# Kernel optimization log

Measured on AMD Instinct MI355X. Metric: run time of the kernel, lower is better.

The kernel has to match this reference:

```python
import jax, jax.numpy as jnp
import numpy as np

B, L, D_MODEL, D_FF, H = 2, 2048, 512, 512, 8
DK = D_FF // H


def _lin(key, fan_in, fan_out):
    k1, k2 = jax.random.split(key)
    lim = 1.0 / np.sqrt(fan_in)
    W = jax.random.uniform(k1, (fan_in, fan_out), jnp.float32, -lim, lim)
    b = jax.random.uniform(k2, (fan_out,), jnp.float32, -lim, lim)
    return W, b


def setup_inputs() -> dict:
    key = jax.random.key(0)
    ks = jax.random.split(key, 13)
    x = jax.random.normal(ks[0], (B, L, D_MODEL), jnp.float32)
    x_knowledge = jax.random.normal(ks[1], (B, L, D_MODEL), jnp.float32)
    Wv, bv = _lin(ks[2], D_MODEL, D_FF)
    Wk, bk = _lin(ks[3], D_MODEL, D_FF)
    Wq, bq = _lin(ks[4], D_MODEL, D_FF)
    Wkf, bkf = _lin(ks[5], D_MODEL, D_FF)
    Wqf, bqf = _lin(ks[6], D_MODEL, D_FF)
    Wq2, bq2 = _lin(ks[7], D_FF, D_FF)
    Wk2, bk2 = _lin(ks[8], D_FF, D_FF)
    Wkf2, bkf2 = _lin(ks[9], D_FF, D_FF)
    Wqf2, bqf2 = _lin(ks[10], D_FF, D_FF)
    Wo, bo = _lin(ks[11], D_FF, D_MODEL)
    return dict(x=x, x_knowledge=x_knowledge, Wv=Wv, bv=bv, Wk=Wk, bk=bk,
                Wq=Wq, bq=bq, Wkf=Wkf, bkf=bkf, Wqf=Wqf, bqf=bqf,
                Wq2=Wq2, bq2=bq2, Wk2=Wk2, bk2=bk2, Wqf2=Wqf2, bqf2=bqf2,
                Wkf2=Wkf2, bkf2=bkf2, Wo=Wo, bo=bo)


def reference(x, x_knowledge, Wv, bv, Wk, bk, Wq, bq, Wkf, bkf, Wqf, bqf,
              Wq2, bq2, Wk2, bk2, Wqf2, bqf2, Wkf2, bkf2, Wo, bo):
    b, l, _ = x.shape
    # first projections from d_model -> d_ff
    v = x @ Wv + bv
    k = x @ Wk + bk
    q = x @ Wq + bq
    k_fei = x_knowledge @ Wkf + bkf
    q_fei = x_knowledge @ Wqf + bqf
    # second projections + NONSTANDARD head split: raw reshape (B,L,d_ff)->(B,h,L,dk)
    q = (q @ Wq2 + bq2).reshape(b, H, l, DK)
    k = (k @ Wk2 + bk2).reshape(b, H, l, DK)
    q_fei = (q_fei @ Wqf2 + bqf2).reshape(b, H, l, DK)
    k_fei = (k_fei @ Wkf2 + bkf2).reshape(b, H, l, DK)
    scale = 1.0 / np.sqrt(2.0 * DK).astype(np.float32)
    att = jnp.einsum('bhld,bhmd->bhlm', q, k) * scale
    att_fei = jnp.einsum('bhld,bhmd->bhlm', q_fei, k_fei) * scale
    score = jax.nn.softmax(att + att_fei, axis=-1)  # dropout is identity at eval
    v = v.reshape(b, H, l, DK)
    out = jnp.einsum('bhlm,bhmd->bhld', score, v).reshape(b, l, D_FF)
    return out @ Wo + bo
```

## Files before the change

kernel.cpp:

```cpp
#include <hip/hip_runtime.h>
#include <hip/hip_bf16.h>

typedef unsigned short u16;
typedef unsigned int   u32;
typedef __attribute__((ext_vector_type(8))) short bf16x8;
typedef __attribute__((ext_vector_type(4))) float f32x4;

#define SCALE 0.08838834764831845f
#define SCLOG 0.12752040542575836f

__device__ inline u16 f2bf(float f) {
  u32 u = __builtin_bit_cast(u32, f);
  u = (u + 0x7FFFu + ((u >> 16) & 1u)) >> 16;
  return (u16)u;
}
__device__ inline float bf2f(u16 b) {
  u32 u = (u32)b << 16;
  return __builtin_bit_cast(float, u);
}

__global__ __launch_bounds__(256) void cvt_bf16(const float* __restrict__ a,
                                                const float* __restrict__ b,
                                                u16* __restrict__ oa,
                                                u16* __restrict__ ob) {
  const float* in = blockIdx.y ? b : a;
  u16* out = blockIdx.y ? ob : oa;
  const int i = (blockIdx.x * 256 + threadIdx.x) * 8;
  float4 f0 = *(const float4*)(in + i);
  float4 f1 = *(const float4*)(in + i + 4);
  alignas(16) u16 t[8] = {f2bf(f0.x), f2bf(f0.y), f2bf(f0.z), f2bf(f0.w),
                          f2bf(f1.x), f2bf(f1.y), f2bf(f1.z), f2bf(f1.w)};
  *(uint4*)(out + i) = *(const uint4*)t;
}

struct TPtrs { const float* p[10]; };

__global__ __launch_bounds__(256) void transposeW(TPtrs ptrs, u16* __restrict__ out) {
  __shared__ u16 ts[64][65];
  const float sc = (blockIdx.z == 5 || blockIdx.z == 7) ? SCLOG : 1.0f;
  const float* in = ptrs.p[blockIdx.z];
  u16* o = out + (size_t)blockIdx.z * 262144;
  const int t = threadIdx.x;
  const int k0 = blockIdx.y * 64, n0 = blockIdx.x * 64;
  for (int pp = 0; pp < 16; ++pp) {
    int id = t + 256 * pp; int r = id >> 6, c = id & 63;
    ts[r][c] = f2bf(in[(size_t)(k0 + r) * 512 + n0 + c] * sc);
  }
  __syncthreads();
  for (int pp = 0; pp < 16; ++pp) {
    int id = t + 256 * pp; int r = id >> 6, c = id & 63;
    o[(size_t)(n0 + r) * 512 + k0 + c] = ts[c][r];
  }
}

struct BPtrs { const float* p[10]; };

__global__ __launch_bounds__(512) void biasPack(BPtrs bp, float* __restrict__ out) {
  const int z = blockIdx.x, n = threadIdx.x;
  const float sc = (z == 5 || z == 7) ? SCLOG : 1.0f;
  out[z * 512 + n] = bp.p[z][n] * sc;
}

__global__ __launch_bounds__(256) void transposeV(const u16* __restrict__ v1,
                                                  u16* __restrict__ vt) {
  __shared__ u16 ts[64][65];
  const size_t base = (size_t)blockIdx.y * 131072;
  const u16* in = v1 + base;
  u16* out = vt + base;
  const int l0 = blockIdx.x * 64;
  const int t = threadIdx.x;
  const int r = t >> 3, c8 = (t & 7) * 8;
  for (int pp = 0; pp < 2; ++pp) {
    int rr = r + pp * 32;
    *(uint4*)&ts[rr][c8] = *(const uint4*)&in[(size_t)(l0 + rr) * 64 + c8];
  }
  __syncthreads();
  for (int pp = 0; pp < 2; ++pp) {
    int d = r + pp * 32;
    alignas(16) u16 tmp[8];
    #pragma unroll
    for (int i = 0; i < 8; ++i) tmp[i] = ts[c8 + i][d];
    *(uint4*)&out[(size_t)d * 2048 + l0 + c8] = *(const uint4*)tmp;
  }
}

struct GemmBatch {
  const u16* A[4];
  const u16* Ax;
  int xsplit;
  void* out[5];
  int wrow0, zstride;
};

template <typename TOUT>
__global__ __launch_bounds__(256, 2) void gemm3(GemmBatch gb,
    const u16* __restrict__ Wt, const float* __restrict__ biasP) {
  const int tx = blockIdx.x, z = blockIdx.z;
  const u16* A = (tx < gb.xsplit) ? gb.A[z] : gb.Ax;
  const int wrow = gb.wrow0 + z * gb.zstride + tx * 128;
  const int m0 = blockIdx.y * 128;
  const u16* B = Wt + (size_t)wrow * 512;
  const float* bias = biasP + wrow;

  const int t = threadIdx.x, wid = t >> 6, lane = t & 63;
  const int lg = lane >> 4, ln = lane & 15;
  const int wr = wid >> 1, wc = wid & 1;

  __shared__ u16 As[2][128][64];
  __shared__ u16 Bs[2][128][64];

  const int srow = t >> 3, sch = t & 7;
  const int sw = (sch ^ (srow & 7)) * 8;
  const u16* Asrc = A + (size_t)(m0 + srow) * 512 + sch * 8;
  const u16* Bsrc = B + (size_t)srow * 512 + sch * 8;

  uint4 ra[4], rb[4];
  #pragma unroll
  for (int p = 0; p < 4; ++p) {
    ra[p] = *(const uint4*)(Asrc + p * 32 * 512);
    rb[p] = *(const uint4*)(Bsrc + p * 32 * 512);
  }
  #pragma unroll
  for (int p = 0; p < 4; ++p) {
    *(uint4*)&As[0][srow + 32 * p][sw] = ra[p];
    *(uint4*)&Bs[0][srow + 32 * p][sw] = rb[p];
  }
  __syncthreads();

  f32x4 acc[4][4];
  #pragma unroll
  for (int i = 0; i < 4; ++i)
    #pragma unroll
    for (int j = 0; j < 4; ++j)
      #pragma unroll
      for (int r = 0; r < 4; ++r) acc[i][j][r] = 0.0f;

  int cur = 0;
  for (int kt = 0; kt < 8; ++kt) {
    if (kt < 7) {
      const int ko = (kt + 1) * 64;
      #pragma unroll
      for (int p = 0; p < 4; ++p) {
        ra[p] = *(const uint4*)(Asrc + ko + p * 32 * 512);
        rb[p] = *(const uint4*)(Bsrc + ko + p * 32 * 512);
      }
    }
    #pragma unroll
    for (int ck = 0; ck < 2; ++ck) {
      bf16x8 af[4], bfr[4];
      #pragma unroll
      for (int mi = 0; mi < 4; ++mi) {
        const int r = wr * 64 + mi * 16 + ln;
        af[mi] = *(const bf16x8*)&As[cur][r][((ck * 4 + lg) ^ (r & 7)) * 8];
      }
      #pragma unroll
      for (int ni = 0; ni < 4; ++ni) {
        const int r = wc * 64 + ni * 16 + ln;
        bfr[ni] = *(const bf16x8*)&Bs[cur][r][((ck * 4 + lg) ^ (r & 7)) * 8];
      }
      #pragma unroll
      for (int mi = 0; mi < 4; ++mi)
        #pragma unroll
        for (int ni = 0; ni < 4; ++ni)
          acc[mi][ni] = __builtin_amdgcn_mfma_f32_16x16x32_bf16(
              af[mi], bfr[ni], acc[mi][ni], 0, 0, 0);
    }
    if (kt < 7) {
      #pragma unroll
      for (int p = 0; p < 4; ++p) {
        *(uint4*)&As[cur ^ 1][srow + 32 * p][sw] = ra[p];
        *(uint4*)&Bs[cur ^ 1][srow + 32 * p][sw] = rb[p];
      }
      __syncthreads();
      cur ^= 1;
    }
  }

  TOUT* C = (TOUT*)gb.out[(wrow >> 9) - (gb.wrow0 >> 9)];
  const int nbase = wrow & 511;
  #pragma unroll
  for (int ni = 0; ni < 4; ++ni) {
    const int colw = wc * 64 + ni * 16 + ln;
    const float bv = bias[colw];
    const int col = nbase + colw;
    #pragma unroll
    for (int mi = 0; mi < 4; ++mi)
      #pragma unroll
      for (int r = 0; r < 4; ++r) {
        const int row = m0 + wr * 64 + mi * 16 + 4 * lg + r;
        const float val = acc[mi][ni][r] + bv;
        if constexpr (sizeof(TOUT) == 4) C[(size_t)row * 512 + col] = val;
        else                             C[(size_t)row * 512 + col] = f2bf(val);
      }
  }
}

__global__ __launch_bounds__(512) void attn5(
    const u16* __restrict__ q2, const u16* __restrict__ k2,
    const u16* __restrict__ qf2, const u16* __restrict__ kf2,
    const u16* __restrict__ vtg, u16* __restrict__ opart,
    float2* __restrict__ mlbuf) {
  const int id = blockIdx.x;
  const int nid = (id & 7) * 32 + (id >> 3);
  const int split = nid & 1;
  const int qt = (nid >> 1) & 7;
  const int bh = nid >> 4;
  const size_t base = (size_t)bh * 131072;
  const int kv0 = split * 1024;

  const u16* Q  = q2  + base;
  const u16* Qf = qf2 + base;
  u16* Op = opart + (size_t)split * 2097152 + base;

  const int t = threadIdx.x, wid = t >> 6, lane = t & 63;
  const int lg = lane >> 4, ln = lane & 15;
  const int r0 = qt * 256 + wid * 32;

  __shared__ u16 K_s [2][64][64];
  __shared__ u16 Kf_s[2][64][64];
  __shared__ u16 Vt_s[2][64][64];
  __shared__ u16 P_s [8][32][64];

  const int srow = t >> 3, sch = t & 7;
  const int sw = (sch ^ (srow & 7)) * 8;
  const u16* Ksrc  = k2  + base + (size_t)(kv0 + srow) * 64 + sch * 8;
  const u16* Kfsrc = kf2 + base + (size_t)(kv0 + srow) * 64 + sch * 8;
  const u16* Vsrc  = vtg + base + (size_t)srow * 2048 + kv0 + sch * 8;

  bf16x8 aq[2][4];
  #pragma unroll
  for (int mi = 0; mi < 2; ++mi) {
    const int row = r0 + mi * 16 + ln;
    aq[mi][0] = *(const bf16x8*)&Q [row * 64 +      lg * 8];
    aq[mi][1] = *(const bf16x8*)&Q [row * 64 + 32 + lg * 8];
    aq[mi][2] = *(const bf16x8*)&Qf[row * 64 +      lg * 8];
    aq[mi][3] = *(const bf16x8*)&Qf[row * 64 + 32 + lg * 8];
  }

  f32x4 oacc[2][4];
  #pragma unroll
  for (int mi = 0; mi < 2; ++mi)
    #pragma unroll
    for (int df = 0; df < 4; ++df)
      #pragma unroll
      for (int r = 0; r < 4; ++r) oacc[mi][df][r] = 0.0f;
  float m_run[2][4], l_par[2][4];
  #pragma unroll
  for (int mi = 0; mi < 2; ++mi)
    #pragma unroll
    for (int r = 0; r < 4; ++r) { m_run[mi][r] = -1e30f; l_par[mi][r] = 0.0f; }

  uint4 rk = *(const uint4*)(Ksrc);
  uint4 rf = *(const uint4*)(Kfsrc);
  uint4 rv = *(const uint4*)(Vsrc);
  *(uint4*)&K_s [0][srow][sw] = rk;
  *(uint4*)&Kf_s[0][srow][sw] = rf;
  *(uint4*)&Vt_s[0][srow][sw] = rv;
  __syncthreads();

  int cur = 0;
  for (int kt = 0; kt < 16; ++kt) {
    if (kt < 15) {
      const int ko = (kt + 1) * 4096;
      rk = *(const uint4*)(Ksrc  + ko);
      rf = *(const uint4*)(Kfsrc + ko);
      rv = *(const uint4*)(Vsrc  + (kt + 1) * 64);
    }

    f32x4 s[2][4];
    #pragma unroll
    for (int cf = 0; cf < 4; ++cf) {
      const int n = cf * 16 + ln;
      const int sx = n & 7;
      bf16x8 b0 = *(const bf16x8*)&K_s [cur][n][((0 + lg) ^ sx) * 8];
      bf16x8 b1 = *(const bf16x8*)&K_s [cur][n][((4 + lg) ^ sx) * 8];
      bf16x8 b2 = *(const bf16x8*)&Kf_s[cur][n][((0 + lg) ^ sx) * 8];
      bf16x8 b3 = *(const bf16x8*)&Kf_s[cur][n][((4 + lg) ^ sx) * 8];
      #pragma unroll
      for (int mi = 0; mi < 2; ++mi) {
        f32x4 a;
        #pragma unroll
        for (int r = 0; r < 4; ++r) a[r] = 0.0f;
        a = __builtin_amdgcn_mfma_f32_16x16x32_bf16(aq[mi][0], b0, a, 0, 0, 0);
        a = __builtin_amdgcn_mfma_f32_16x16x32_bf16(aq[mi][1], b1, a, 0, 0, 0);
        a = __builtin_amdgcn_mfma_f32_16x16x32_bf16(aq[mi][2], b2, a, 0, 0, 0);
        a = __builtin_amdgcn_mfma_f32_16x16x32_bf16(aq[mi][3], b3, a, 0, 0, 0);
        s[mi][cf] = a;
      }
    }

    float smax[2][4];
    bool viol = false;
    #pragma unroll
    for (int mi = 0; mi < 2; ++mi)
      #pragma unroll
      for (int r = 0; r < 4; ++r) {
        smax[mi][r] = fmaxf(fmaxf(s[mi][0][r], s[mi][1][r]),
                            fmaxf(s[mi][2][r], s[mi][3][r]));
        viol = viol || (smax[mi][r] > m_run[mi][r] + 11.0f);
      }
    if (__any(viol)) {
      #pragma unroll
      for (int off = 1; off < 16; off <<= 1)
        #pragma unroll
        for (int mi = 0; mi < 2; ++mi)
          #pragma unroll
          for (int r = 0; r < 4; ++r)
            smax[mi][r] = fmaxf(smax[mi][r], __shfl_xor(smax[mi][r], off, 64));
      #pragma unroll
      for (int mi = 0; mi < 2; ++mi)
        #pragma unroll
        for (int r = 0; r < 4; ++r) {
          const float mnew = fmaxf(m_run[mi][r], smax[mi][r]);
          const float corr = exp2f(m_run[mi][r] - mnew);
          m_run[mi][r] = mnew;
          l_par[mi][r] *= corr;
          #pragma unroll
          for (int df = 0; df < 4; ++df) oacc[mi][df][r] *= corr;
        }
    }
    #pragma unroll
    for (int mi = 0; mi < 2; ++mi)
      #pragma unroll
      for (int cf = 0; cf < 4; ++cf) {
        const int col = cf * 16 + ln;
        #pragma unroll
        for (int r = 0; r < 4; ++r) {
          const int rr = 4 * lg + r;
          const float p = exp2f(s[mi][cf][r] - m_run[mi][r]);
          l_par[mi][r] += p;
          P_s[wid][mi * 16 + rr][col ^ ((rr & 7) * 8)] =
              __builtin_bit_cast(u16, __float2bfloat16(p));
        }
      }

    #pragma unroll
    for (int kc = 0; kc < 2; ++kc) {
      const int kk = kc * 32 + lg * 8;
      bf16x8 ap0 = *(const bf16x8*)&P_s[wid][ln]     [kk ^ ((ln & 7) * 8)];
      bf16x8 ap1 = *(const bf16x8*)&P_s[wid][16 + ln][kk ^ ((ln & 7) * 8)];
      #pragma unroll
      for (int df = 0; df < 4; ++df) {
        const int n = df * 16 + ln;
        bf16x8 bv = *(const bf16x8*)&Vt_s[cur][n][((kc * 4 + lg) ^ (n & 7)) * 8];
        oacc[0][df] = __builtin_amdgcn_mfma_f32_16x16x32_bf16(ap0, bv, oacc[0][df], 0, 0, 0);
        oacc[1][df] = __builtin_amdgcn_mfma_f32_16x16x32_bf16(ap1, bv, oacc[1][df], 0, 0, 0);
      }
    }

    if (kt < 15) {
      *(uint4*)&K_s [cur ^ 1][srow][sw] = rk;
      *(uint4*)&Kf_s[cur ^ 1][srow][sw] = rf;
      *(uint4*)&Vt_s[cur ^ 1][srow][sw] = rv;
      __syncthreads();
      cur ^= 1;
    }
  }

  #pragma unroll
  for (int off = 1; off < 16; off <<= 1)
    #pragma unroll
    for (int mi = 0; mi < 2; ++mi)
      #pragma unroll
      for (int r = 0; r < 4; ++r)
        l_par[mi][r] += __shfl_xor(l_par[mi][r], off, 64);

  #pragma unroll
  for (int mi = 0; mi < 2; ++mi)
    #pragma unroll
    for (int df = 0; df < 4; ++df)
      #pragma unroll
      for (int r = 0; r < 4; ++r) {
        const int row = r0 + mi * 16 + 4 * lg + r;
        const int col = df * 16 + ln;
        Op[(size_t)row * 64 + col] = f2bf(oacc[mi][df][r]);
      }
  if (ln == 0) {
    #pragma unroll
    for (int mi = 0; mi < 2; ++mi)
      #pragma unroll
      for (int r = 0; r < 4; ++r) {
        const int grow = bh * 2048 + r0 + mi * 16 + 4 * lg + r;
        mlbuf[split * 32768 + grow] = make_float2(m_run[mi][r], l_par[mi][r]);
      }
  }
}

__global__ __launch_bounds__(256) void combine(
    const u16* __restrict__ opart, const float2* __restrict__ mlbuf,
    u16* __restrict__ att) {
  const int gid = blockIdx.x * 256 + threadIdx.x;
  const int row = gid >> 3, c8 = (gid & 7) * 8;
  const float2 ml1 = mlbuf[row];
  const float2 ml2 = mlbuf[32768 + row];
  const float mx = fmaxf(ml1.x, ml2.x);
  const float a1 = exp2f(ml1.x - mx), a2 = exp2f(ml2.x - mx);
  const float inv = 1.0f / (ml1.y * a1 + ml2.y * a2);
  const float w1 = a1 * inv, w2 = a2 * inv;
  uint4 o1 = *(const uint4*)&opart[(size_t)row * 64 + c8];
  uint4 o2 = *(const uint4*)&opart[2097152 + (size_t)row * 64 + c8];
  const u16* p1 = (const u16*)&o1;
  const u16* p2 = (const u16*)&o2;
  alignas(16) u16 ot[8];
  #pragma unroll
  for (int i = 0; i < 8; ++i)
    ot[i] = f2bf(bf2f(p1[i]) * w1 + bf2f(p2[i]) * w2);
  *(uint4*)&att[(size_t)row * 64 + c8] = *(const uint4*)ot;
}

extern "C" void kernel_launch(void* const* d_in, const int* in_sizes, int n_in,
                              void* d_out, int out_size, void* d_ws, size_t ws_size,
                              hipStream_t stream) {
  const float* x    = (const float*)d_in[0];
  const float* xk   = (const float*)d_in[1];
  const float* Wv   = (const float*)d_in[2];  const float* bv   = (const float*)d_in[3];
  const float* Wk   = (const float*)d_in[4];  const float* bk   = (const float*)d_in[5];
  const float* Wq   = (const float*)d_in[6];  const float* bq   = (const float*)d_in[7];
  const float* Wkf  = (const float*)d_in[8];  const float* bkf  = (const float*)d_in[9];
  const float* Wqf  = (const float*)d_in[10]; const float* bqf  = (const float*)d_in[11];
  const float* Wq2  = (const float*)d_in[12]; const float* bq2  = (const float*)d_in[13];
  const float* Wk2  = (const float*)d_in[14]; const float* bk2  = (const float*)d_in[15];
  const float* Wqf2 = (const float*)d_in[16]; const float* bqf2 = (const float*)d_in[17];
  const float* Wkf2 = (const float*)d_in[18]; const float* bkf2 = (const float*)d_in[19];
  const float* Wo   = (const float*)d_in[20]; const float* bo   = (const float*)d_in[21];

  u16* ws = (u16*)d_ws;
  u16* Wt = ws;
  float* biasP = (float*)(ws + 2621440);
  u16* bufs = ws + 2621440 + 10240;
  const size_t BUF = 2097152;
  u16* v1  = bufs + 0 * BUF;
  u16* k1  = bufs + 1 * BUF;
  u16* q1  = bufs + 2 * BUF;
  u16* kf1 = bufs + 3 * BUF;
  u16* qf1 = bufs + 4 * BUF;
  u16* q2  = bufs + 5 * BUF;
  u16* k2  = bufs + 6 * BUF;
  u16* qf2 = bufs + 7 * BUF;
  u16* kf2 = bufs + 8 * BUF;
  float2* mlbuf = (float2*)(bufs + 9 * BUF);

  cvt_bf16<<<dim3(1024, 2), 256, 0, stream>>>(x, xk, q2, k2);

  TPtrs tp;
  tp.p[0] = Wv;  tp.p[1] = Wk;  tp.p[2] = Wq;   tp.p[3] = Wkf;  tp.p[4] = Wqf;
  tp.p[5] = Wq2; tp.p[6] = Wk2; tp.p[7] = Wqf2; tp.p[8] = Wkf2; tp.p[9] = Wo;
  transposeW<<<dim3(8, 8, 10), 256, 0, stream>>>(tp, Wt);

  BPtrs bp;
  bp.p[0] = bv;  bp.p[1] = bk;  bp.p[2] = bq;   bp.p[3] = bkf;  bp.p[4] = bqf;
  bp.p[5] = bq2; bp.p[6] = bk2; bp.p[7] = bqf2; bp.p[8] = bkf2; bp.p[9] = bo;
  biasPack<<<dim3(10), 512, 0, stream>>>(bp, biasP);

  GemmBatch g1 = {};
  g1.A[0] = q2;  g1.Ax = k2;  g1.xsplit = 12;
  g1.out[0] = v1; g1.out[1] = k1; g1.out[2] = q1; g1.out[3] = kf1; g1.out[4] = qf1;
  g1.wrow0 = 0; g1.zstride = 0;
  gemm3<u16><<<dim3(20, 32, 1), 256, 0, stream>>>(g1, Wt, biasP);

  GemmBatch g3 = {};
  g3.A[0] = q1; g3.A[1] = k1; g3.A[2] = qf1; g3.A[3] = kf1;
  g3.Ax = q1; g3.xsplit = 100;
  g3.out[0] = q2; g3.out[1] = k2; g3.out[2] = qf2; g3.out[3] = kf2;
  g3.wrow0 = 2560; g3.zstride = 512;
  gemm3<u16><<<dim3(4, 32, 4), 256, 0, stream>>>(g3, Wt, biasP);

  transposeV<<<dim3(32, 16), 256, 0, stream>>>(v1, q1);

  attn5<<<dim3(256), 512, 0, stream>>>(q2, k2, qf2, kf2, q1, kf1, mlbuf);

  combine<<<dim3(1024), 256, 0, stream>>>(kf1, mlbuf, v1);

  GemmBatch g4 = {};
  g4.A[0] = v1; g4.Ax = v1; g4.xsplit = 100;
  g4.out[0] = d_out;
  g4.wrow0 = 4608; g4.zstride = 0;
  gemm3<float><<<dim3(4, 32, 1), 256, 0, stream>>>(g4, Wt, biasP);
}
```

Measured before the change: 119.2 us.

## Use direct global-to-LDS loads in GEMM and split attention KV four ways

The GEMM now loads tiles straight into LDS with global_load_lds and uses a single buffer. It drops the register staging, the XOR swizzle and the double buffering, and raises launch bounds to 4 blocks per CU. The attention kernel splits the KV range four ways instead of two, doubling the grid to 512 blocks, and drops its shared-memory double buffer. The combine kernel now merges four partials. The aim is more occupancy and parallelism, traded against losing load/compute overlap, possible LDS bank conflicts from the unswizzled layout, and extra partial-output traffic.

```diff
diff --git a/kernel.cpp b/kernel.cpp
--- a/kernel.cpp
+++ b/kernel.cpp
@@ -17,6 +17,12 @@
 __device__ inline float bf2f(u16 b) {
   u32 u = (u32)b << 16;
   return __builtin_bit_cast(float, u);
+}
+
+__device__ __forceinline__ void glds16(const u16* g, u16* l) {
+  __builtin_amdgcn_global_load_lds(
+      (__attribute__((address_space(1))) void*)g,
+      (__attribute__((address_space(3))) void*)l, 16, 0, 0);
 }
 
 __global__ __launch_bounds__(256) void cvt_bf16(const float* __restrict__ a,
@@ -93,7 +99,7 @@
 };
 
 template <typename TOUT>
-__global__ __launch_bounds__(256, 2) void gemm3(GemmBatch gb,
+__global__ __launch_bounds__(256, 4) void gemm4(GemmBatch gb,
     const u16* __restrict__ Wt, const float* __restrict__ biasP) {
   const int tx = blockIdx.x, z = blockIdx.z;
   const u16* A = (tx < gb.xsplit) ? gb.A[z] : gb.Ax;
@@ -106,26 +112,11 @@
   const int lg = lane >> 4, ln = lane & 15;
   const int wr = wid >> 1, wc = wid & 1;
 
-  __shared__ u16 As[2][128][64];
-  __shared__ u16 Bs[2][128][64];
-
-  const int srow = t >> 3, sch = t & 7;
-  const int sw = (sch ^ (srow & 7)) * 8;
-  const u16* Asrc = A + (size_t)(m0 + srow) * 512 + sch * 8;
-  const u16* Bsrc = B + (size_t)srow * 512 + sch * 8;
-
-  uint4 ra[4], rb[4];
-  #pragma unroll
-  for (int p = 0; p < 4; ++p) {
-    ra[p] = *(const uint4*)(Asrc + p * 32 * 512);
-    rb[p] = *(const uint4*)(Bsrc + p * 32 * 512);
-  }
-  #pragma unroll
-  for (int p = 0; p < 4; ++p) {
-    *(uint4*)&As[0][srow + 32 * p][sw] = ra[p];
-    *(uint4*)&Bs[0][srow + 32 * p][sw] = rb[p];
-  }
-  __syncthreads();
+  __shared__ u16 As[128][64];
+  __shared__ u16 Bs[128][64];
+
+  const u16* Ag = A + (size_t)m0 * 512;
+  const int lrow = lane >> 3, lch = lane & 7;
 
   f32x4 acc[4][4];
   #pragma unroll
@@ -135,29 +126,25 @@
       #pragma unroll
       for (int r = 0; r < 4; ++r) acc[i][j][r] = 0.0f;
 
-  int cur = 0;
   for (int kt = 0; kt < 8; ++kt) {
-    if (kt < 7) {
-      const int ko = (kt + 1) * 64;
-      #pragma unroll
-      for (int p = 0; p < 4; ++p) {
-        ra[p] = *(const uint4*)(Asrc + ko + p * 32 * 512);
-        rb[p] = *(const uint4*)(Bsrc + ko + p * 32 * 512);
-      }
-    }
+    #pragma unroll
+    for (int c = 0; c < 4; ++c) {
+      const int row = (wid * 4 + c) * 8 + lrow;
+      const size_t go = (size_t)row * 512 + kt * 64 + lch * 8;
+      glds16(Ag + go, &As[(wid * 4 + c) * 8][0]);
+      glds16(B  + go, &Bs[(wid * 4 + c) * 8][0]);
+    }
+    __syncthreads();
+
     #pragma unroll
     for (int ck = 0; ck < 2; ++ck) {
       bf16x8 af[4], bfr[4];
       #pragma unroll
-      for (int mi = 0; mi < 4; ++mi) {
-        const int r = wr * 64 + mi * 16 + ln;
-        af[mi] = *(const bf16x8*)&As[cur][r][((ck * 4 + lg) ^ (r & 7)) * 8];
-      }
-      #pragma unroll
-      for (int ni = 0; ni < 4; ++ni) {
-        const int r = wc * 64 + ni * 16 + ln;
-        bfr[ni] = *(const bf16x8*)&Bs[cur][r][((ck * 4 + lg) ^ (r & 7)) * 8];
-      }
+      for (int mi = 0; mi < 4; ++mi)
+        af[mi] = *(const bf16x8*)&As[wr * 64 + mi * 16 + ln][ck * 32 + lg * 8];
+      #pragma unroll
+      for (int ni = 0; ni < 4; ++ni)
+        bfr[ni] = *(const bf16x8*)&Bs[wc * 64 + ni * 16 + ln][ck * 32 + lg * 8];
       #pragma unroll
       for (int mi = 0; mi < 4; ++mi)
         #pragma unroll
@@ -165,15 +152,7 @@
           acc[mi][ni] = __builtin_amdgcn_mfma_f32_16x16x32_bf16(
               af[mi], bfr[ni], acc[mi][ni], 0, 0, 0);
     }
-    if (kt < 7) {
-      #pragma unroll
-      for (int p = 0; p < 4; ++p) {
-        *(uint4*)&As[cur ^ 1][srow + 32 * p][sw] = ra[p];
-        *(uint4*)&Bs[cur ^ 1][srow + 32 * p][sw] = rb[p];
-      }
-      __syncthreads();
-      cur ^= 1;
-    }
+    if (kt < 7) __syncthreads();
   }
 
   TOUT* C = (TOUT*)gb.out[(wrow >> 9) - (gb.wrow0 >> 9)];
@@ -195,30 +174,32 @@
   }
 }
 
-__global__ __launch_bounds__(512) void attn5(
+struct OPtrs { u16* o0; u16* o1; u16* o2; u16* o3; float2* ml; };
+
+__global__ __launch_bounds__(512) void attn6(
     const u16* __restrict__ q2, const u16* __restrict__ k2,
     const u16* __restrict__ qf2, const u16* __restrict__ kf2,
-    const u16* __restrict__ vtg, u16* __restrict__ opart,
-    float2* __restrict__ mlbuf) {
+    const u16* __restrict__ vtg, OPtrs op) {
   const int id = blockIdx.x;
-  const int nid = (id & 7) * 32 + (id >> 3);
-  const int split = nid & 1;
-  const int qt = (nid >> 1) & 7;
-  const int bh = nid >> 4;
+  const int nid = (id & 7) * 64 + (id >> 3);
+  const int split = nid & 3;
+  const int qt = (nid >> 2) & 7;
+  const int bh = nid >> 5;
   const size_t base = (size_t)bh * 131072;
-  const int kv0 = split * 1024;
+  const int kv0 = split * 512;
 
   const u16* Q  = q2  + base;
   const u16* Qf = qf2 + base;
-  u16* Op = opart + (size_t)split * 2097152 + base;
+  u16* Op = ((split == 0) ? op.o0 : (split == 1) ? op.o1 :
+             (split == 2) ? op.o2 : op.o3) + base;
 
   const int t = threadIdx.x, wid = t >> 6, lane = t & 63;
   const int lg = lane >> 4, ln = lane & 15;
   const int r0 = qt * 256 + wid * 32;
 
-  __shared__ u16 K_s [2][64][64];
-  __shared__ u16 Kf_s[2][64][64];
-  __shared__ u16 Vt_s[2][64][64];
+  __shared__ u16 K_s [64][64];
+  __shared__ u16 Kf_s[64][64];
+  __shared__ u16 Vt_s[64][64];
   __shared__ u16 P_s [8][32][64];
 
   const int srow = t >> 3, sch = t & 7;
@@ -253,14 +234,13 @@
   uint4 rk = *(const uint4*)(Ksrc);
   uint4 rf = *(const uint4*)(Kfsrc);
   uint4 rv = *(const uint4*)(Vsrc);
-  *(uint4*)&K_s [0][srow][sw] = rk;
-  *(uint4*)&Kf_s[0][srow][sw] = rf;
-  *(uint4*)&Vt_s[0][srow][sw] = rv;
+  *(uint4*)&K_s [srow][sw] = rk;
+  *(uint4*)&Kf_s[srow][sw] = rf;
+  *(uint4*)&Vt_s[srow][sw] = rv;
   __syncthreads();
 
-  int cur = 0;
-  for (int kt = 0; kt < 16; ++kt) {
-    if (kt < 15) {
+  for (int kt = 0; kt < 8; ++kt) {
+    if (kt < 7) {
       const int ko = (kt + 1) * 4096;
       rk = *(const uint4*)(Ksrc  + ko);
       rf = *(const uint4*)(Kfsrc + ko);
@@ -272,10 +252,10 @@
     for (int cf = 0; cf < 4; ++cf) {
       const int n = cf * 16 + ln;
       const int sx = n & 7;
-      bf16x8 b0 = *(const bf16x8*)&K_s [cur][n][((0 + lg) ^ sx) * 8];
-      bf16x8 b1 = *(const bf16x8*)&K_s [cur][n][((4 + lg) ^ sx) * 8];
-      bf16x8 b2 = *(const bf16x8*)&Kf_s[cur][n][((0 + lg) ^ sx) * 8];
-      bf16x8 b3 = *(const bf16x8*)&Kf_s[cur][n][((4 + lg) ^ sx) * 8];
+      bf16x8 b0 = *(const bf16x8*)&K_s [n][((0 + lg) ^ sx) * 8];
+      bf16x8 b1 = *(const bf16x8*)&K_s [n][((4 + lg) ^ sx) * 8];
+      bf16x8 b2 = *(const bf16x8*)&Kf_s[n][((0 + lg) ^ sx) * 8];
+      bf16x8 b3 = *(const bf16x8*)&Kf_s[n][((4 + lg) ^ sx) * 8];
       #pragma unroll
       for (int mi = 0; mi < 2; ++mi) {
         f32x4 a;
@@ -342,18 +322,18 @@
       #pragma unroll
       for (int df = 0; df < 4; ++df) {
         const int n = df * 16 + ln;
-        bf16x8 bv = *(const bf16x8*)&Vt_s[cur][n][((kc * 4 + lg) ^ (n & 7)) * 8];
+        bf16x8 bv = *(const bf16x8*)&Vt_s[n][((kc * 4 + lg) ^ (n & 7)) * 8];
         oacc[0][df] = __builtin_amdgcn_mfma_f32_16x16x32_bf16(ap0, bv, oacc[0][df], 0, 0, 0);
         oacc[1][df] = __builtin_amdgcn_mfma_f32_16x16x32_bf16(ap1, bv, oacc[1][df], 0, 0, 0);
       }
     }
 
-    if (kt < 15) {
-      *(uint4*)&K_s [cur ^ 1][srow][sw] = rk;
-      *(uint4*)&Kf_s[cur ^ 1][srow][sw] = rf;
-      *(uint4*)&Vt_s[cur ^ 1][srow][sw] = rv;
+    __syncthreads();
+    if (kt < 7) {
+      *(uint4*)&K_s [srow][sw] = rk;
+      *(uint4*)&Kf_s[srow][sw] = rf;
+      *(uint4*)&Vt_s[srow][sw] = rv;
       __syncthreads();
-      cur ^= 1;
     }
   }
 
@@ -381,31 +361,41 @@
       #pragma unroll
       for (int r = 0; r < 4; ++r) {
         const int grow = bh * 2048 + r0 + mi * 16 + 4 * lg + r;
-        mlbuf[split * 32768 + grow] = make_float2(m_run[mi][r], l_par[mi][r]);
-      }
-  }
-}
-
-__global__ __launch_bounds__(256) void combine(
-    const u16* __restrict__ opart, const float2* __restrict__ mlbuf,
-    u16* __restrict__ att) {
+        op.ml[split * 32768 + grow] = make_float2(m_run[mi][r], l_par[mi][r]);
+      }
+  }
+}
+
+__global__ __launch_bounds__(256) void combine4(
+    const u16* __restrict__ o0, const u16* __restrict__ o1,
+    const u16* __restrict__ o2, const u16* __restrict__ o3,
+    const float2* __restrict__ ml, u16* __restrict__ att) {
   const int gid = blockIdx.x * 256 + threadIdx.x;
   const int row = gid >> 3, c8 = (gid & 7) * 8;
-  const float2 ml1 = mlbuf[row];
-  const float2 ml2 = mlbuf[32768 + row];
-  const float mx = fmaxf(ml1.x, ml2.x);
-  const float a1 = exp2f(ml1.x - mx), a2 = exp2f(ml2.x - mx);
-  const float inv = 1.0f / (ml1.y * a1 + ml2.y * a2);
-  const float w1 = a1 * inv, w2 = a2 * inv;
-  uint4 o1 = *(const uint4*)&opart[(size_t)row * 64 + c8];
-  uint4 o2 = *(const uint4*)&opart[2097152 + (size_t)row * 64 + c8];
-  const u16* p1 = (const u16*)&o1;
-  const u16* p2 = (const u16*)&o2;
+  const float2 m0 = ml[row];
+  const float2 m1 = ml[32768 + row];
+  const float2 m2 = ml[65536 + row];
+  const float2 m3 = ml[98304 + row];
+  const float mx = fmaxf(fmaxf(m0.x, m1.x), fmaxf(m2.x, m3.x));
+  const float a0 = exp2f(m0.x - mx), a1 = exp2f(m1.x - mx);
+  const float a2 = exp2f(m2.x - mx), a3 = exp2f(m3.x - mx);
+  const float inv = 1.0f / (m0.y * a0 + m1.y * a1 + m2.y * a2 + m3.y * a3);
+  const float w0 = a0 * inv, w1 = a1 * inv, w2 = a2 * inv, w3 = a3 * inv;
+  const size_t o = (size_t)row * 64 + c8;
+  uint4 v0 = *(const uint4*)&o0[o];
+  uint4 v1 = *(const uint4*)&o1[o];
+  uint4 v2 = *(const uint4*)&o2[o];
+  uint4 v3 = *(const uint4*)&o3[o];
+  const u16* p0 = (const u16*)&v0;
+  const u16* p1 = (const u16*)&v1;
+  const u16* p2 = (const u16*)&v2;
+  const u16* p3 = (const u16*)&v3;
   alignas(16) u16 ot[8];
   #pragma unroll
   for (int i = 0; i < 8; ++i)
-    ot[i] = f2bf(bf2f(p1[i]) * w1 + bf2f(p2[i]) * w2);
-  *(uint4*)&att[(size_t)row * 64 + c8] = *(const uint4*)ot;
+    ot[i] = f2bf(bf2f(p0[i]) * w0 + bf2f(p1[i]) * w1 +
+                 bf2f(p2[i]) * w2 + bf2f(p3[i]) * w3);
+  *(uint4*)&att[o] = *(const uint4*)ot;
 }
 
 extern "C" void kernel_launch(void* const* d_in, const int* in_sizes, int n_in,
@@ -438,7 +428,8 @@
   u16* k2  = bufs + 6 * BUF;
   u16* qf2 = bufs + 7 * BUF;
   u16* kf2 = bufs + 8 * BUF;
-  float2* mlbuf = (float2*)(bufs + 9 * BUF);
+  u16* op3 = bufs + 9 * BUF;
+  float2* mlbuf = (float2*)(bufs + 10 * BUF);
 
   cvt_bf16<<<dim3(1024, 2), 256, 0, stream>>>(x, xk, q2, k2);
 
@@ -456,24 +447,26 @@
   g1.A[0] = q2;  g1.Ax = k2;  g1.xsplit = 12;
   g1.out[0] = v1; g1.out[1] = k1; g1.out[2] = q1; g1.out[3] = kf1; g1.out[4] = qf1;
   g1.wrow0 = 0; g1.zstride = 0;
-  gemm3<u16><<<dim3(20, 32, 1), 256, 0, stream>>>(g1, Wt, biasP);
+  gemm4<u16><<<dim3(20, 32, 1), 256, 0, stream>>>(g1, Wt, biasP);
 
   GemmBatch g3 = {};
   g3.A[0] = q1; g3.A[1] = k1; g3.A[2] = qf1; g3.A[3] = kf1;
   g3.Ax = q1; g3.xsplit = 100;
   g3.out[0] = q2; g3.out[1] = k2; g3.out[2] = qf2; g3.out[3] = kf2;
   g3.wrow0 = 2560; g3.zstride = 512;
-  gemm3<u16><<<dim3(4, 32, 4), 256, 0, stream>>>(g3, Wt, biasP);
+  gemm4<u16><<<dim3(4, 32, 4), 256, 0, stream>>>(g3, Wt, biasP);
 
   transposeV<<<dim3(32, 16), 256, 0, stream>>>(v1, q1);
 
-  attn5<<<dim3(256), 512, 0, stream>>>(q2, k2, qf2, kf2, q1, kf1, mlbuf);
-
-  combine<<<dim3(1024), 256, 0, stream>>>(kf1, mlbuf, v1);
+  OPtrs op;
+  op.o0 = kf1; op.o1 = qf1; op.o2 = k1; op.o3 = op3; op.ml = mlbuf;
+  attn6<<<dim3(512), 512, 0, stream>>>(q2, k2, qf2, kf2, q1, op);
+
+  combine4<<<dim3(1024), 256, 0, stream>>>(kf1, qf1, k1, op3, mlbuf, v1);
 
   GemmBatch g4 = {};
   g4.A[0] = v1; g4.Ax = v1; g4.xsplit = 100;
   g4.out[0] = d_out;
   g4.wrow0 = 4608; g4.zstride = 0;
-  gemm3<float><<<dim3(4, 32, 1), 256, 0, stream>>>(g4, Wt, biasP);
-}
+  gemm4<float><<<dim3(4, 32, 1), 256, 0, stream>>>(g4, Wt, biasP);
+}
```

Result: slower. 125.2 us (+5.0%).
